# Kernel tuning notes

Measured on AMD Instinct MI355X. Metric: run time of the kernel, lower is better.

Reference implementation:

```python
import jax, jax.numpy as jnp
import numpy as np

HIDDEN_DIM = 128
NUM_HEADS = 4
B, S = 16, 1024
NEG = -1e9
EPS = 1e-5


def setup_inputs() -> dict:
    key = jax.random.key(0)
    ks = jax.random.split(key, 6)
    D, H = HIDDEN_DIM, NUM_HEADS
    x = jax.random.normal(ks[0], (B, S, D), dtype=jnp.float32)
    edge_type_matrix = jax.random.randint(ks[1], (S, S), 0, 5, dtype=jnp.int64)
    scale = 0.02
    W_in = jax.random.normal(ks[2], (H, 3 * D, D), dtype=jnp.float32) * scale   # per-head in_proj_weight
    b_in = jax.random.normal(ks[3], (H, 3 * D), dtype=jnp.float32) * scale      # per-head in_proj_bias
    W_out = jax.random.normal(ks[4], (H, D, D), dtype=jnp.float32) * scale      # per-head out_proj.weight
    b_out = jax.random.normal(ks[5], (H, D), dtype=jnp.float32) * scale         # per-head out_proj.bias
    return {"x": x, "edge_type_matrix": edge_type_matrix,
            "W_in": W_in, "b_in": b_in, "W_out": W_out, "b_out": b_out}


def reference(x, edge_type_matrix, W_in, b_in, W_out, b_out):
    Bx, Sx, D = x.shape
    H = W_in.shape[0]
    # F.layer_norm(x, x.size()[1:]): normalize jointly over (S, D), no affine
    mu = jnp.mean(x, axis=(1, 2), keepdims=True)
    var = jnp.mean(jnp.square(x - mu), axis=(1, 2), keepdims=True)
    xn = (x - mu) / jnp.sqrt(var + EPS)
    # all heads' qkv in one contraction: [b,h,s,3D]
    qkv = jnp.einsum('bsd,hed->bhse', xn, W_in) + b_in[None, :, None, :]
    q, k, v = jnp.split(qkv, 3, axis=-1)                      # each [b,h,s,D]
    scores = jnp.einsum('bhsd,bhtd->bhst', q, k) / jnp.sqrt(jnp.float32(D))
    # additive mask per head: 0 where edge_type == head_id(1..H), else -1e9
    head_ids = jnp.arange(1, H + 1, dtype=edge_type_matrix.dtype)
    mask = jnp.where(edge_type_matrix[None, :, :] == head_ids[:, None, None],
                     jnp.float32(0.0), jnp.float32(NEG))       # [h,s,s]
    attn = jax.nn.softmax(scores + mask[None], axis=-1)
    ctx = jnp.einsum('bhst,bhtd->bhsd', attn, v)
    # torch out_proj: ctx @ W.T + b
    out_h = jnp.einsum('bhsd,hed->bhse', ctx, W_out) + b_out[None, :, None, :]
    # dropout p=0.05 is identity in eval mode; concat heads on feature dim
    out = jnp.transpose(out_h, (0, 2, 1, 3)).reshape(Bx, Sx, H * D)
    return out


if __name__ == '__main__':
    inp = setup_inputs()
    y = reference(**inp)
    print(y.shape)
```

## Files before the change

### kernel.cpp

```cpp
#include <hip/hip_runtime.h>
#include <math.h>

static constexpr int Dh = 128;
static constexpr int NH = 4;
static constexpr int NB = 16;
static constexpr int SS = 1024;
static constexpr float NEGF = -1e9f;
static constexpr float SCALE = 0.08838834764831843f;

typedef short s16x8 __attribute__((ext_vector_type(8)));
typedef float f32x4 __attribute__((ext_vector_type(4)));

#define MFMA32(a, b, c) __builtin_amdgcn_mfma_f32_16x16x32_bf16(a, b, c, 0, 0, 0)

__device__ inline ushort f2bf(float f) {
    union { float f; unsigned u; } v; v.f = f;
    unsigned r = v.u + 0x7FFFu + ((v.u >> 16) & 1u);
    return (ushort)(r >> 16);
}

__global__ __launch_bounds__(256) void ln_part_kernel(const float* __restrict__ x,
                                                      float* __restrict__ part) {
    const int b = blockIdx.x >> 4, p = blockIdx.x & 15;
    const int tid = threadIdx.x;
    const float4* xb = (const float4*)(x + (size_t)b * SS * Dh) + p * 2048;
    float s = 0.f, ss = 0.f;
    for (int i = tid; i < 2048; i += 256) {
        float4 v = xb[i];
        s  += v.x + v.y + v.z + v.w;
        ss += v.x * v.x + v.y * v.y + v.z * v.z + v.w * v.w;
    }
    __shared__ float r1[256], r2[256];
    r1[tid] = s; r2[tid] = ss;
    __syncthreads();
    for (int off = 128; off > 0; off >>= 1) {
        if (tid < off) { r1[tid] += r1[tid + off]; r2[tid] += r2[tid + off]; }
        __syncthreads();
    }
    if (tid == 0) { part[blockIdx.x * 2] = r1[0]; part[blockIdx.x * 2 + 1] = r2[0]; }
}

__global__ __launch_bounds__(256) void maskbit_prep_kernel(const int* __restrict__ edge,
                                                           unsigned long long* __restrict__ mbit) {
    const int idx = blockIdx.x * 256 + threadIdx.x;
    const int s = idx >> 4, w = idx & 15;
    const int4* ep = (const int4*)(edge + (size_t)s * SS + w * 64);
    unsigned long long m0 = 0, m1 = 0, m2 = 0, m3 = 0;
    #pragma unroll
    for (int j = 0; j < 16; ++j) {
        int4 e = ep[j];
        const int base = j * 4;
        m0 |= (e.x == 1) ? (1ull << (base + 0)) : 0ull;
        m1 |= (e.x == 2) ? (1ull << (base + 0)) : 0ull;
        m2 |= (e.x == 3) ? (1ull << (base + 0)) : 0ull;
        m3 |= (e.x == 4) ? (1ull << (base + 0)) : 0ull;
        m0 |= (e.y == 1) ? (1ull << (base + 1)) : 0ull;
        m1 |= (e.y == 2) ? (1ull << (base + 1)) : 0ull;
        m2 |= (e.y == 3) ? (1ull << (base + 1)) : 0ull;
        m3 |= (e.y == 4) ? (1ull << (base + 1)) : 0ull;
        m0 |= (e.z == 1) ? (1ull << (base + 2)) : 0ull;
        m1 |= (e.z == 2) ? (1ull << (base + 2)) : 0ull;
        m2 |= (e.z == 3) ? (1ull << (base + 2)) : 0ull;
        m3 |= (e.z == 4) ? (1ull << (base + 2)) : 0ull;
        m0 |= (e.w == 1) ? (1ull << (base + 3)) : 0ull;
        m1 |= (e.w == 2) ? (1ull << (base + 3)) : 0ull;
        m2 |= (e.w == 3) ? (1ull << (base + 3)) : 0ull;
        m3 |= (e.w == 4) ? (1ull << (base + 3)) : 0ull;
    }
    mbit[((size_t)0 * SS + s) * 16 + w] = m0;
    mbit[((size_t)1 * SS + s) * 16 + w] = m1;
    mbit[((size_t)2 * SS + s) * 16 + w] = m2;
    mbit[((size_t)3 * SS + s) * 16 + w] = m3;
}

__global__ __launch_bounds__(256) void qkv_mfma_kernel(const float* __restrict__ x,
                                                       const float* __restrict__ w,
                                                       const float* __restrict__ bias,
                                                       const float* __restrict__ part,
                                                       ushort* __restrict__ qo,
                                                       ushort* __restrict__ ko,
                                                       ushort* __restrict__ vto) {
    __shared__ ushort smem[2 * 128 * 72];
    ushort* As = smem;
    ushort* Bs = smem + 128 * 72;
    ushort* Rs = smem;
    const int tid = threadIdx.x, wave = tid >> 6, lane = tid & 63;
    const int lrow = lane & 15, quad = lane >> 4;
    const int wm = wave & 1, wn = wave >> 1;
    const int col0 = blockIdx.x * 128;
    const int row0 = blockIdx.y * 128;
    const int bb = row0 >> 10;

    float s_ = 0.f, ss_ = 0.f;
    #pragma unroll
    for (int p = 0; p < 16; ++p) { s_ += part[(bb * 16 + p) * 2]; ss_ += part[(bb * 16 + p) * 2 + 1]; }
    const float invN = 1.0f / (float)(SS * Dh);
    const float mu = s_ * invN;
    const float rstd = 1.0f / sqrtf(ss_ * invN - mu * mu + 1e-5f);

    f32x4 acc[4][4];
    #pragma unroll
    for (int mi = 0; mi < 4; ++mi)
        #pragma unroll
        for (int ni = 0; ni < 4; ++ni) acc[mi][ni] = (f32x4){0.f, 0.f, 0.f, 0.f};

    for (int kk = 0; kk < 128; kk += 64) {
        if (kk) __syncthreads();
        #pragma unroll
        for (int p = 0; p < 8; ++p) {
            int slot = p * 256 + tid;
            int r = slot >> 4, c4 = (slot & 15) << 2;
            float4 v = *(const float4*)(x + (size_t)(row0 + r) * Dh + kk + c4);
            ushort4 pa;
            pa.x = f2bf((v.x - mu) * rstd); pa.y = f2bf((v.y - mu) * rstd);
            pa.z = f2bf((v.z - mu) * rstd); pa.w = f2bf((v.w - mu) * rstd);
            *(ushort4*)&As[r * 72 + c4] = pa;
            float4 wv = *(const float4*)(w + (size_t)(col0 + r) * Dh + kk + c4);
            ushort4 pb;
            pb.x = f2bf(wv.x); pb.y = f2bf(wv.y); pb.z = f2bf(wv.z); pb.w = f2bf(wv.w);
            *(ushort4*)&Bs[r * 72 + c4] = pb;
        }
        __syncthreads();
        #pragma unroll
        for (int kc = 0; kc < 2; ++kc) {
            s16x8 af[4], bf[4];
            #pragma unroll
            for (int mi = 0; mi < 4; ++mi)
                af[mi] = *(const s16x8*)&As[(wm * 64 + 16 * mi + lrow) * 72 + kc * 32 + quad * 8];
            #pragma unroll
            for (int ni = 0; ni < 4; ++ni)
                bf[ni] = *(const s16x8*)&Bs[(wn * 64 + 16 * ni + lrow) * 72 + kc * 32 + quad * 8];
            #pragma unroll
            for (int mi = 0; mi < 4; ++mi)
                #pragma unroll
                for (int ni = 0; ni < 4; ++ni)
                    acc[mi][ni] = MFMA32(af[mi], bf[ni], acc[mi][ni]);
        }
    }

    const int seg = col0 % 384, typ = seg >> 7, h = col0 / 384;
    const size_t bh = (size_t)bb * NH + h;
    const int sl_blk = row0 & 1023;
    float bia[4];
    #pragma unroll
    for (int ni = 0; ni < 4; ++ni) bia[ni] = bias[col0 + wn * 64 + 16 * ni + lrow];
    const float sc = (typ == 0) ? SCALE : 1.f;

    __syncthreads();
    if (typ < 2) {
        #pragma unroll
        for (int mi = 0; mi < 4; ++mi)
            #pragma unroll
            for (int ni = 0; ni < 4; ++ni)
                #pragma unroll
                for (int reg = 0; reg < 4; ++reg)
                    Rs[(wm * 64 + 16 * mi + quad * 4 + reg) * 136 + wn * 64 + 16 * ni + lrow]
                        = f2bf((acc[mi][ni][reg] + bia[ni]) * sc);
    } else {
        #pragma unroll
        for (int mi = 0; mi < 4; ++mi)
            #pragma unroll
            for (int ni = 0; ni < 4; ++ni) {
                ushort4 pk;
                pk.x = f2bf(acc[mi][ni][0] + bia[ni]);
                pk.y = f2bf(acc[mi][ni][1] + bia[ni]);
                pk.z = f2bf(acc[mi][ni][2] + bia[ni]);
                pk.w = f2bf(acc[mi][ni][3] + bia[ni]);
                *(ushort4*)&Rs[(wn * 64 + 16 * ni + lrow) * 136 + wm * 64 + 16 * mi + quad * 4] = pk;
            }
    }
    __syncthreads();

    ushort* dstb;
    int pitch;
    if (typ == 0)      { dstb = qo  + bh * SS * 128 + (size_t)sl_blk * 128; pitch = 128; }
    else if (typ == 1) { dstb = ko  + bh * SS * 128 + (size_t)sl_blk * 128; pitch = 128; }
    else               { dstb = vto + bh * (size_t)128 * SS + sl_blk;       pitch = SS;  }
    #pragma unroll
    for (int p = 0; p < 8; ++p) {
        int slot = p * 256 + tid;
        int r = slot >> 4, c8 = (slot & 15) * 8;
        *(s16x8*)&dstb[(size_t)r * pitch + c8] = *(const s16x8*)&Rs[r * 136 + c8];
    }
}

static constexpr int KS_LD = 136;
static constexpr int VT_LD = 72;
static constexpr int PS_LD = 72;
static constexpr int WS_LD = 136;
static constexpr int OS_LD = 136;
static constexpr int SMEM_N = 26112;

__global__ __launch_bounds__(256, 2) void attn_fused_kernel(const ushort* __restrict__ qg_,
                                                            const ushort* __restrict__ kg_,
                                                            const ushort* __restrict__ vg_,
                                                            const unsigned long long* __restrict__ mbit,
                                                            const float* __restrict__ wo,
                                                            const float* __restrict__ bo,
                                                            float* __restrict__ out) {
    const int qt = blockIdx.x, h = blockIdx.y, b = blockIdx.z;
    const int s0 = qt * 128;
    const int tid = threadIdx.x;
    const int wave = tid >> 6, lane = tid & 63;
    const int lrow = lane & 15, quad = lane >> 4;

    __shared__ ushort smem[SMEM_N];
    ushort* Ks  = smem;
    ushort* Vt  = smem + 64 * KS_LD;
    ushort* Psw = smem + 64 * KS_LD + 128 * VT_LD + wave * 16 * PS_LD;
    ushort* Osl = smem + wave * 16 * OS_LD;
    ushort* Ws  = smem + 4 * 16 * OS_LD;

    const size_t bh = (size_t)(b * NH + h);
    const ushort* qg = qg_ + bh * SS * 128;
    const ushort* kg = kg_ + bh * SS * 128;
    const ushort* vg = vg_ + bh * 128 * SS;
    const unsigned long long* mrow0 = mbit + ((size_t)h * SS + (s0 + 32 * wave + lrow)) * 16;
    const unsigned long long* mrow1 = mrow0 + 16 * 16;

    s16x8 qf[2][4];
    #pragma unroll
    for (int g = 0; g < 2; ++g) {
        const ushort* qr = qg + (size_t)(s0 + 32 * wave + 16 * g + lrow) * 128 + quad * 8;
        #pragma unroll
        for (int kc = 0; kc < 4; ++kc) qf[g][kc] = *(const s16x8*)(qr + kc * 32);
    }

    s16x8 kreg[4], vreg[4];
    #pragma unroll
    for (int p = 0; p < 4; ++p) {
        int slot = p * 256 + tid;
        int r = slot >> 4, c = (slot & 15) * 8;
        kreg[p] = *(const s16x8*)(kg + (size_t)r * 128 + c);
    }
    #pragma unroll
    for (int p = 0; p < 4; ++p) {
        int slot = p * 256 + tid;
        int r = slot >> 3, c = (slot & 7) * 8;
        vreg[p] = *(const s16x8*)(vg + (size_t)r * SS + c);
    }

    f32x4 oacc[2][8];
    #pragma unroll
    for (int g = 0; g < 2; ++g)
        #pragma unroll
        for (int nb = 0; nb < 8; ++nb) oacc[g][nb] = (f32x4){0.f, 0.f, 0.f, 0.f};
    float m_run[2] = {-INFINITY, -INFINITY};
    float l_run[2] = {0.f, 0.f};

    for (int kt = 0; kt < 16; ++kt) {
        const int t0 = kt * 64;
        unsigned long long mw0 = mrow0[kt];
        unsigned long long mw1 = mrow1[kt];

        __syncthreads();
        #pragma unroll
        for (int p = 0; p < 4; ++p) {
            int slot = p * 256 + tid;
            int r = slot >> 4, c = (slot & 15) * 8;
            *(s16x8*)&Ks[r * KS_LD + c] = kreg[p];
        }
        #pragma unroll
        for (int p = 0; p < 4; ++p) {
            int slot = p * 256 + tid;
            int r = slot >> 3, c = (slot & 7) * 8;
            *(s16x8*)&Vt[r * VT_LD + c] = vreg[p];
        }
        __syncthreads();

        if (kt < 15) {
            const int t1 = t0 + 64;
            #pragma unroll
            for (int p = 0; p < 4; ++p) {
                int slot = p * 256 + tid;
                int r = slot >> 4, c = (slot & 15) * 8;
                kreg[p] = *(const s16x8*)(kg + (size_t)(t1 + r) * 128 + c);
            }
            #pragma unroll
            for (int p = 0; p < 4; ++p) {
                int slot = p * 256 + tid;
                int r = slot >> 3, c = (slot & 7) * 8;
                vreg[p] = *(const s16x8*)(vg + (size_t)r * SS + t1 + c);
            }
        }

        f32x4 sacc[2][4];
        #pragma unroll
        for (int g = 0; g < 2; ++g)
            #pragma unroll
            for (int cb = 0; cb < 4; ++cb) sacc[g][cb] = (f32x4){0.f, 0.f, 0.f, 0.f};
        #pragma unroll
        for (int cb = 0; cb < 4; ++cb) {
            s16x8 kf[4];
            #pragma unroll
            for (int kc = 0; kc < 4; ++kc)
                kf[kc] = *(const s16x8*)&Ks[(16 * cb + lrow) * KS_LD + kc * 32 + quad * 8];
            #pragma unroll
            for (int g = 0; g < 2; ++g)
                #pragma unroll
                for (int kc = 0; kc < 4; ++kc)
                    sacc[g][cb] = MFMA32(kf[kc], qf[g][kc], sacc[g][cb]);
        }

        s16x8 af[2][2];
        #pragma unroll
        for (int g = 0; g < 2; ++g) {
            const unsigned long long mw = g ? mw1 : mw0;
            float sv[4][4];
            float tm = -INFINITY;
            #pragma unroll
            for (int cb = 0; cb < 4; ++cb) {
                unsigned nib = (unsigned)(mw >> (16 * cb + quad * 4)) & 0xFu;
                #pragma unroll
                for (int r = 0; r < 4; ++r) {
                    sv[cb][r] = (nib & (1u << r)) ? sacc[g][cb][r] : NEGF;
                    tm = fmaxf(tm, sv[cb][r]);
                }
            }
            tm = fmaxf(tm, __shfl_xor(tm, 16));
            tm = fmaxf(tm, __shfl_xor(tm, 32));
            float mn = fmaxf(m_run[g], tm);
            float al = __expf(m_run[g] - mn);
            float rs = 0.f;
            #pragma unroll
            for (int cb = 0; cb < 4; ++cb) {
                float p0 = __expf(sv[cb][0] - mn);
                float p1 = __expf(sv[cb][1] - mn);
                float p2 = __expf(sv[cb][2] - mn);
                float p3 = __expf(sv[cb][3] - mn);
                rs += (p0 + p1) + (p2 + p3);
                ushort4 pw;
                pw.x = f2bf(p0); pw.y = f2bf(p1); pw.z = f2bf(p2); pw.w = f2bf(p3);
                *(ushort4*)&Psw[lrow * PS_LD + 16 * cb + quad * 4] = pw;
            }
            rs += __shfl_xor(rs, 16);
            rs += __shfl_xor(rs, 32);
            l_run[g] = l_run[g] * al + rs;
            m_run[g] = mn;
            float alT[4];
            #pragma unroll
            for (int r = 0; r < 4; ++r) alT[r] = __shfl(al, quad * 4 + r);
            #pragma unroll
            for (int nb = 0; nb < 8; ++nb)
                #pragma unroll
                for (int r = 0; r < 4; ++r) oacc[g][nb][r] *= alT[r];
            #pragma unroll
            for (int kc = 0; kc < 2; ++kc)
                af[g][kc] = *(const s16x8*)&Psw[lrow * PS_LD + kc * 32 + quad * 8];
        }

        #pragma unroll
        for (int nb = 0; nb < 8; ++nb) {
            #pragma unroll
            for (int kc = 0; kc < 2; ++kc) {
                s16x8 bf = *(const s16x8*)&Vt[(16 * nb + lrow) * VT_LD + kc * 32 + quad * 8];
                #pragma unroll
                for (int g = 0; g < 2; ++g)
                    oacc[g][nb] = MFMA32(af[g][kc], bf, oacc[g][nb]);
            }
        }
    }

    __syncthreads();
    const float* wbase = wo + (size_t)h * Dh * Dh;
    #pragma unroll
    for (int p = 0; p < 16; ++p) {
        int slot = p * 256 + tid;
        int r = slot >> 5, c4 = (slot & 31) << 2;
        float4 wv = *(const float4*)(wbase + (size_t)r * Dh + c4);
        ushort4 pb;
        pb.x = f2bf(wv.x); pb.y = f2bf(wv.y); pb.z = f2bf(wv.z); pb.w = f2bf(wv.w);
        *(ushort4*)&Ws[r * WS_LD + c4] = pb;
    }
    s16x8 afo[2][4];
    #pragma unroll
    for (int g = 0; g < 2; ++g) {
        float inv = 1.0f / l_run[g];
        float invT[4];
        #pragma unroll
        for (int r = 0; r < 4; ++r) invT[r] = __shfl(inv, quad * 4 + r);
        #pragma unroll
        for (int nb = 0; nb < 8; ++nb)
            #pragma unroll
            for (int r = 0; r < 4; ++r)
                Osl[(quad * 4 + r) * OS_LD + 16 * nb + lrow] = f2bf(oacc[g][nb][r] * invT[r]);
        #pragma unroll
        for (int kc = 0; kc < 4; ++kc)
            afo[g][kc] = *(const s16x8*)&Osl[lrow * OS_LD + kc * 32 + quad * 8];
    }
    __syncthreads();

    const size_t orow0 = (size_t)b * SS + s0 + 32 * wave;
    #pragma unroll
    for (int nb = 0; nb < 8; ++nb) {
        float bia = bo[h * Dh + nb * 16 + lrow];
        f32x4 facc[2];
        facc[0] = (f32x4){0.f, 0.f, 0.f, 0.f};
        facc[1] = (f32x4){0.f, 0.f, 0.f, 0.f};
        #pragma unroll
        for (int kc = 0; kc < 4; ++kc) {
            s16x8 wf = *(const s16x8*)&Ws[(16 * nb + lrow) * WS_LD + kc * 32 + quad * 8];
            facc[0] = MFMA32(afo[0][kc], wf, facc[0]);
            facc[1] = MFMA32(afo[1][kc], wf, facc[1]);
        }
        #pragma unroll
        for (int g = 0; g < 2; ++g)
            #pragma unroll
            for (int reg = 0; reg < 4; ++reg) {
                size_t m = orow0 + 16 * g + quad * 4 + reg;
                out[m * (NH * Dh) + h * Dh + nb * 16 + lrow] = facc[g][reg] + bia;
            }
    }
}

extern "C" void kernel_launch(void* const* d_in, const int* in_sizes, int n_in,
                              void* d_out, int out_size, void* d_ws, size_t ws_size,
                              hipStream_t stream) {
    const float* x     = (const float*)d_in[0];
    const int*   edge  = (const int*)d_in[1];
    const float* w_in  = (const float*)d_in[2];
    const float* b_in  = (const float*)d_in[3];
    const float* w_out = (const float*)d_in[4];
    const float* b_out = (const float*)d_in[5];
    float* out = (float*)d_out;

    float* ws   = (float*)d_ws;
    float* part = ws;
    unsigned long long* mbit = (unsigned long long*)(ws + 1024);
    ushort* qo  = (ushort*)(mbit + (size_t)NH * SS * 16);
    const size_t QSZ = (size_t)NB * NH * SS * 128;
    ushort* ko  = qo + QSZ;
    ushort* vto = ko + QSZ;

    ln_part_kernel<<<256, 256, 0, stream>>>(x, part);
    maskbit_prep_kernel<<<SS * 16 / 256, 256, 0, stream>>>(edge, mbit);
    qkv_mfma_kernel<<<dim3(12, 128), 256, 0, stream>>>(x, w_in, b_in, part, qo, ko, vto);
    attn_fused_kernel<<<dim3(SS / 128, NH, NB), 256, 0, stream>>>(qo, ko, vto, mbit, w_out, b_out, out);
}
```

Measured before the change: 181.5 us.

## Keep softmax probabilities in registers via transposed PV MFMA, merge prep kernels

The PV product is recomputed as O^T = V^T·P^T with the 16x16x16 bf16 MFMA, so the score accumulator layout feeds P straight from registers. This removes the LDS round-trip for P and the per-row alpha shuffles. The LayerNorm partial-sum and mask-bit kernels are merged into one launch, and the attention grid is reordered so batch-head varies fastest. The trade-off is twice as many MFMA instructions, each with half the K depth, and a transposed accumulator layout that the epilogue now writes out with packed stores.

```diff
diff --git a/kernel.cpp b/kernel.cpp
--- a/kernel.cpp
+++ b/kernel.cpp
@@ -9,9 +9,11 @@
 static constexpr float SCALE = 0.08838834764831843f;
 
 typedef short s16x8 __attribute__((ext_vector_type(8)));
+typedef short s16x4 __attribute__((ext_vector_type(4)));
 typedef float f32x4 __attribute__((ext_vector_type(4)));
 
 #define MFMA32(a, b, c) __builtin_amdgcn_mfma_f32_16x16x32_bf16(a, b, c, 0, 0, 0)
+#define MFMA16(a, b, c) __builtin_amdgcn_mfma_f32_16x16x16bf16_1k(a, b, c, 0, 0, 0)
 
 __device__ inline ushort f2bf(float f) {
     union { float f; unsigned u; } v; v.f = f;
@@ -19,8 +21,10 @@
     return (ushort)(r >> 16);
 }
 
-__global__ __launch_bounds__(256) void ln_part_kernel(const float* __restrict__ x,
-                                                      float* __restrict__ part) {
+__global__ __launch_bounds__(256) void ln_mask_kernel(const float* __restrict__ x,
+                                                      float* __restrict__ part,
+                                                      const int* __restrict__ edge,
+                                                      unsigned long long* __restrict__ mbit) {
     const int b = blockIdx.x >> 4, p = blockIdx.x & 15;
     const int tid = threadIdx.x;
     const float4* xb = (const float4*)(x + (size_t)b * SS * Dh) + p * 2048;
@@ -38,39 +42,38 @@
         __syncthreads();
     }
     if (tid == 0) { part[blockIdx.x * 2] = r1[0]; part[blockIdx.x * 2 + 1] = r2[0]; }
-}
-
-__global__ __launch_bounds__(256) void maskbit_prep_kernel(const int* __restrict__ edge,
-                                                           unsigned long long* __restrict__ mbit) {
-    const int idx = blockIdx.x * 256 + threadIdx.x;
-    const int s = idx >> 4, w = idx & 15;
-    const int4* ep = (const int4*)(edge + (size_t)s * SS + w * 64);
-    unsigned long long m0 = 0, m1 = 0, m2 = 0, m3 = 0;
-    #pragma unroll
-    for (int j = 0; j < 16; ++j) {
-        int4 e = ep[j];
-        const int base = j * 4;
-        m0 |= (e.x == 1) ? (1ull << (base + 0)) : 0ull;
-        m1 |= (e.x == 2) ? (1ull << (base + 0)) : 0ull;
-        m2 |= (e.x == 3) ? (1ull << (base + 0)) : 0ull;
-        m3 |= (e.x == 4) ? (1ull << (base + 0)) : 0ull;
-        m0 |= (e.y == 1) ? (1ull << (base + 1)) : 0ull;
-        m1 |= (e.y == 2) ? (1ull << (base + 1)) : 0ull;
-        m2 |= (e.y == 3) ? (1ull << (base + 1)) : 0ull;
-        m3 |= (e.y == 4) ? (1ull << (base + 1)) : 0ull;
-        m0 |= (e.z == 1) ? (1ull << (base + 2)) : 0ull;
-        m1 |= (e.z == 2) ? (1ull << (base + 2)) : 0ull;
-        m2 |= (e.z == 3) ? (1ull << (base + 2)) : 0ull;
-        m3 |= (e.z == 4) ? (1ull << (base + 2)) : 0ull;
-        m0 |= (e.w == 1) ? (1ull << (base + 3)) : 0ull;
-        m1 |= (e.w == 2) ? (1ull << (base + 3)) : 0ull;
-        m2 |= (e.w == 3) ? (1ull << (base + 3)) : 0ull;
-        m3 |= (e.w == 4) ? (1ull << (base + 3)) : 0ull;
-    }
-    mbit[((size_t)0 * SS + s) * 16 + w] = m0;
-    mbit[((size_t)1 * SS + s) * 16 + w] = m1;
-    mbit[((size_t)2 * SS + s) * 16 + w] = m2;
-    mbit[((size_t)3 * SS + s) * 16 + w] = m3;
+
+    if (blockIdx.x < 64) {
+        const int idx = blockIdx.x * 256 + tid;
+        const int sr = idx >> 4, w = idx & 15;
+        const int4* ep = (const int4*)(edge + (size_t)sr * SS + w * 64);
+        unsigned long long m0 = 0, m1 = 0, m2 = 0, m3 = 0;
+        #pragma unroll
+        for (int j = 0; j < 16; ++j) {
+            int4 e = ep[j];
+            const int base = j * 4;
+            m0 |= (e.x == 1) ? (1ull << (base + 0)) : 0ull;
+            m1 |= (e.x == 2) ? (1ull << (base + 0)) : 0ull;
+            m2 |= (e.x == 3) ? (1ull << (base + 0)) : 0ull;
+            m3 |= (e.x == 4) ? (1ull << (base + 0)) : 0ull;
+            m0 |= (e.y == 1) ? (1ull << (base + 1)) : 0ull;
+            m1 |= (e.y == 2) ? (1ull << (base + 1)) : 0ull;
+            m2 |= (e.y == 3) ? (1ull << (base + 1)) : 0ull;
+            m3 |= (e.y == 4) ? (1ull << (base + 1)) : 0ull;
+            m0 |= (e.z == 1) ? (1ull << (base + 2)) : 0ull;
+            m1 |= (e.z == 2) ? (1ull << (base + 2)) : 0ull;
+            m2 |= (e.z == 3) ? (1ull << (base + 2)) : 0ull;
+            m3 |= (e.z == 4) ? (1ull << (base + 2)) : 0ull;
+            m0 |= (e.w == 1) ? (1ull << (base + 3)) : 0ull;
+            m1 |= (e.w == 2) ? (1ull << (base + 3)) : 0ull;
+            m2 |= (e.w == 3) ? (1ull << (base + 3)) : 0ull;
+            m3 |= (e.w == 4) ? (1ull << (base + 3)) : 0ull;
+        }
+        mbit[((size_t)0 * SS + sr) * 16 + w] = m0;
+        mbit[((size_t)1 * SS + sr) * 16 + w] = m1;
+        mbit[((size_t)2 * SS + sr) * 16 + w] = m2;
+        mbit[((size_t)3 * SS + sr) * 16 + w] = m3;
+    }
 }
 
 __global__ __launch_bounds__(256) void qkv_mfma_kernel(const float* __restrict__ x,
@@ -186,7 +189,6 @@
 
 static constexpr int KS_LD = 136;
 static constexpr int VT_LD = 72;
-static constexpr int PS_LD = 72;
 static constexpr int WS_LD = 136;
 static constexpr int OS_LD = 136;
 static constexpr int SMEM_N = 26112;
@@ -198,7 +200,8 @@
                                                             const float* __restrict__ wo,
                                                             const float* __restrict__ bo,
                                                             float* __restrict__ out) {
-    const int qt = blockIdx.x, h = blockIdx.y, b = blockIdx.z;
+    const int bhi = blockIdx.x, qt = blockIdx.y;
+    const int b = bhi >> 2, h = bhi & 3;
     const int s0 = qt * 128;
     const int tid = threadIdx.x;
     const int wave = tid >> 6, lane = tid & 63;
@@ -207,7 +210,6 @@
     __shared__ ushort smem[SMEM_N];
     ushort* Ks  = smem;
     ushort* Vt  = smem + 64 * KS_LD;
-    ushort* Psw = smem + 64 * KS_LD + 128 * VT_LD + wave * 16 * PS_LD;
     ushort* Osl = smem + wave * 16 * OS_LD;
     ushort* Ws  = smem + 4 * 16 * OS_LD;
 
@@ -302,7 +304,7 @@
                     sacc[g][cb] = MFMA32(kf[kc], qf[g][kc], sacc[g][cb]);
         }
 
-        s16x8 af[2][2];
+        s16x4 pf[2][4];
         #pragma unroll
         for (int g = 0; g < 2; ++g) {
             const unsigned long long mw = g ? mw1 : mw0;
@@ -329,34 +331,29 @@
                 float p2 = __expf(sv[cb][2] - mn);
                 float p3 = __expf(sv[cb][3] - mn);
                 rs += (p0 + p1) + (p2 + p3);
-                ushort4 pw;
-                pw.x = f2bf(p0); pw.y = f2bf(p1); pw.z = f2bf(p2); pw.w = f2bf(p3);
-                *(ushort4*)&Psw[lrow * PS_LD + 16 * cb + quad * 4] = pw;
+                s16x4 pk;
+                pk[0] = (short)f2bf(p0); pk[1] = (short)f2bf(p1);
+                pk[2] = (short)f2bf(p2); pk[3] = (short)f2bf(p3);
+                pf[g][cb] = pk;
             }
             rs += __shfl_xor(rs, 16);
             rs += __shfl_xor(rs, 32);
             l_run[g] = l_run[g] * al + rs;
             m_run[g] = mn;
-            float alT[4];
-            #pragma unroll
-            for (int r = 0; r < 4; ++r) alT[r] = __shfl(al, quad * 4 + r);
             #pragma unroll
             for (int nb = 0; nb < 8; ++nb)
                 #pragma unroll
-                for (int r = 0; r < 4; ++r) oacc[g][nb][r] *= alT[r];
-            #pragma unroll
-            for (int kc = 0; kc < 2; ++kc)
-                af[g][kc] = *(const s16x8*)&Psw[lrow * PS_LD + kc * 32 + quad * 8];
+                for (int r = 0; r < 4; ++r) oacc[g][nb][r] *= al;
         }
 
         #pragma unroll
         for (int nb = 0; nb < 8; ++nb) {
             #pragma unroll
-            for (int kc = 0; kc < 2; ++kc) {
-                s16x8 bf = *(const s16x8*)&Vt[(16 * nb + lrow) * VT_LD + kc * 32 + quad * 8];
+            for (int kb = 0; kb < 4; ++kb) {
+                s16x4 vf = *(const s16x4*)&Vt[(16 * nb + lrow) * VT_LD + kb * 16 + quad * 4];
                 #pragma unroll
                 for (int g = 0; g < 2; ++g)
-                    oacc[g][nb] = MFMA32(af[g][kc], bf, oacc[g][nb]);
+                    oacc[g][nb] = MFMA16(vf, pf[g][kb], oacc[g][nb]);
             }
         }
     }
@@ -376,14 +373,15 @@
     #pragma unroll
     for (int g = 0; g < 2; ++g) {
         float inv = 1.0f / l_run[g];
-        float invT[4];
-        #pragma unroll
-        for (int r = 0; r < 4; ++r) invT[r] = __shfl(inv, quad * 4 + r);
-        #pragma unroll
-        for (int nb = 0; nb < 8; ++nb)
-            #pragma unroll
-            for (int r = 0; r < 4; ++r)
-                Osl[(quad * 4 + r) * OS_LD + 16 * nb + lrow] = f2bf(oacc[g][nb][r] * invT[r]);
+        #pragma unroll
+        for (int nb = 0; nb < 8; ++nb) {
+            ushort4 pk;
+            pk.x = f2bf(oacc[g][nb][0] * inv);
+            pk.y = f2bf(oacc[g][nb][1] * inv);
+            pk.z = f2bf(oacc[g][nb][2] * inv);
+            pk.w = f2bf(oacc[g][nb][3] * inv);
+            *(ushort4*)&Osl[lrow * OS_LD + 16 * nb + quad * 4] = pk;
+        }
         #pragma unroll
         for (int kc = 0; kc < 4; ++kc)
             afo[g][kc] = *(const s16x8*)&Osl[lrow * OS_LD + kc * 32 + quad * 8];
@@ -432,8 +430,7 @@
     ushort* ko  = qo + QSZ;
     ushort* vto = ko + QSZ;
 
-    ln_part_kernel<<<256, 256, 0, stream>>>(x, part);
-    maskbit_prep_kernel<<<SS * 16 / 256, 256, 0, stream>>>(edge, mbit);
+    ln_mask_kernel<<<256, 256, 0, stream>>>(x, part, edge, mbit);
     qkv_mfma_kernel<<<dim3(12, 128), 256, 0, stream>>>(x, w_in, b_in, part, qo, ko, vto);
-    attn_fused_kernel<<<dim3(SS / 128, NH, NB), 256, 0, stream>>>(qo, ko, vto, mbit, w_out, b_out, out);
+    attn_fused_kernel<<<dim3(NB * NH, SS / 128), 256, 0, stream>>>(qo, ko, vto, mbit, w_out, b_out, out);
 }
```

Result: faster. 174.8 us (-3.7%).
